# Performance work log

Hardware: AMD Instinct MI355X
Metric: run time of the kernel (lower is better)

## Reference

```python
import jax, jax.numpy as jnp
import numpy as np

N_NODES = 100000
N_EDGES = 1000000
IN_CH = 128
OUT_CH = 128
T_DIM = 64


def setup_inputs() -> dict:
    key = jax.random.key(0)
    ks = jax.random.split(key, 9)
    x = jax.random.normal(ks[0], (N_NODES, IN_CH), dtype=jnp.float32)
    edge_index = jax.random.randint(ks[1], (2, N_EDGES), 0, N_NODES, dtype=jnp.int64)
    temporal_features = jax.random.normal(ks[2], (N_EDGES, T_DIM), dtype=jnp.float32)
    # Learned params (torch nn.Linear convention: weight [out, in], bias [out])
    s = 1.0 / np.sqrt(IN_CH)
    st = 1.0 / np.sqrt(T_DIM)
    W_S_w = jax.random.uniform(ks[3], (OUT_CH, IN_CH), minval=-s, maxval=s, dtype=jnp.float32)
    W_S_b = jax.random.uniform(ks[4], (OUT_CH,), minval=-s, maxval=s, dtype=jnp.float32)
    W_T_w = jax.random.uniform(ks[5], (OUT_CH, IN_CH), minval=-s, maxval=s, dtype=jnp.float32)
    W_T_b = jax.random.uniform(ks[6], (OUT_CH,), minval=-s, maxval=s, dtype=jnp.float32)
    T_w = jax.random.uniform(ks[7], (OUT_CH, T_DIM), minval=-st, maxval=st, dtype=jnp.float32)
    T_b = jax.random.uniform(ks[8], (OUT_CH,), minval=-st, maxval=st, dtype=jnp.float32)
    return {
        "x": x, "edge_index": edge_index, "temporal_features": temporal_features,
        "W_S_w": W_S_w, "W_S_b": W_S_b, "W_T_w": W_T_w, "W_T_b": W_T_b,
        "T_w": T_w, "T_b": T_b,
    }


def reference(x, edge_index, temporal_features, W_S_w, W_S_b, W_T_w, W_T_b, T_w, T_b):
    num_nodes = x.shape[0]
    row, col = edge_index[0], edge_index[1]
    # self transform: [N, out]
    self_features = x @ W_S_w.T + W_S_b
    # gather neighbor feats then transform: [E, out]
    neighbor_features = x[col] @ W_T_w.T + W_T_b
    # temporal encodings: [E, out]
    temporal_encodings = temporal_features @ T_w.T + T_b
    messages = neighbor_features + temporal_encodings
    # scatter-add aggregation over destination nodes
    aggregated = jax.ops.segment_sum(messages, row, num_segments=num_nodes)
    return jax.nn.relu(self_features + aggregated)
```

## Files before the change

kernel.cpp:

```cpp
#include <hip/hip_runtime.h>

#define N_NODES 100000
#define M_PAD   100096
#define N_EDGES 1000000
#define K_TOT   320
#define NCHUNK  98

#define BM  128
#define LDA 72

#define XCONV_THREADS 1600000

typedef __attribute__((ext_vector_type(8))) short bf16x8;
typedef __attribute__((ext_vector_type(4))) float f32x4;

__device__ __forceinline__ unsigned short f2bf(float f) {
    unsigned u = __float_as_uint(f);
    u += 0x7FFFu + ((u >> 16) & 1u);
    return (unsigned short)(u >> 16);
}
__device__ __forceinline__ unsigned pack2(float a, float b) {
    return (unsigned)f2bf(a) | ((unsigned)f2bf(b) << 16);
}

__global__ __launch_bounds__(256) void prep_kernel(
        const float* __restrict__ x,
        const float* __restrict__ WSw,
        const float* __restrict__ WTw,
        const float* __restrict__ Tw,
        const float* __restrict__ WTb,
        const float* __restrict__ Tb,
        unsigned short* __restrict__ xb,
        unsigned short* __restrict__ Gtb,
        float* __restrict__ bias2) {
    int gid = blockIdx.x * 256 + threadIdx.x;
    if (gid < XCONV_THREADS) {
        const float4* p = (const float4*)x + (size_t)gid * 2;
        float4 u0 = p[0], u1 = p[1];
        uint4 w;
        w.x = pack2(u0.x, u0.y);
        w.y = pack2(u0.z, u0.w);
        w.z = pack2(u1.x, u1.y);
        w.w = pack2(u1.z, u1.w);
        *(uint4*)(xb + (size_t)gid * 8) = w;
    } else {
        int idx = gid - XCONV_THREADS;
        if (idx < K_TOT * 128) {
            int k = idx >> 7;
            int o = idx & 127;
            float v = (k < 128) ? WSw[o * 128 + k]
                    : (k < 256) ? WTw[o * 128 + (k - 128)]
                                : Tw[o * 64 + (k - 256)];
            Gtb[(size_t)o * K_TOT + k] = f2bf(v);
        }
        if (idx < 128) bias2[idx] = WTb[idx] + Tb[idx];
    }
}

__global__ __launch_bounds__(256) void hist_kernel(const int* __restrict__ ei,
                                                   int* __restrict__ hist) {
    int e = blockIdx.x * 256 + threadIdx.x;
    if (e < N_EDGES) atomicAdd(&hist[ei[e]], 1);
}

__global__ __launch_bounds__(256) void scan_pass1(const int* __restrict__ hist,
                                                  int* __restrict__ chunksum) {
    __shared__ int ts[256];
    int b = blockIdx.x, t = threadIdx.x;
    int i = b * 1024 + t * 4;
    int s = 0;
#pragma unroll
    for (int j = 0; j < 4; ++j)
        if (i + j < N_NODES) s += hist[i + j];
    ts[t] = s;
    __syncthreads();
    for (int off = 128; off > 0; off >>= 1) {
        if (t < off) ts[t] += ts[t + off];
        __syncthreads();
    }
    if (t == 0) chunksum[b] = ts[0];
}

__global__ __launch_bounds__(128) void scan_mid(const int* __restrict__ chunksum,
                                                int* __restrict__ chunkoff) {
    __shared__ int ts[128];
    int t = threadIdx.x;
    int v = (t < NCHUNK) ? chunksum[t] : 0;
    ts[t] = v;
    __syncthreads();
    for (int off = 1; off < 128; off <<= 1) {
        int a = (t >= off) ? ts[t - off] : 0;
        __syncthreads();
        ts[t] += a;
        __syncthreads();
    }
    if (t < NCHUNK) chunkoff[t] = ts[t] - v;
}

__global__ __launch_bounds__(256) void scan_pass2(const int* __restrict__ hist,
                                                  const int* __restrict__ chunkoff,
                                                  int* __restrict__ offsets) {
    __shared__ int ts[256];
    int b = blockIdx.x, t = threadIdx.x;
    int i0 = b * 1024 + t * 4;
    int v[4];
    int s = 0;
#pragma unroll
    for (int j = 0; j < 4; ++j) {
        v[j] = (i0 + j < N_NODES) ? hist[i0 + j] : 0;
        s += v[j];
    }
    ts[t] = s;
    __syncthreads();
    for (int off = 1; off < 256; off <<= 1) {
        int add = (t >= off) ? ts[t - off] : 0;
        __syncthreads();
        ts[t] += add;
        __syncthreads();
    }
    int run = chunkoff[b] + ts[t] - s;
#pragma unroll
    for (int j = 0; j < 4; ++j) {
        if (i0 + j < N_NODES) offsets[i0 + j] = run;
        run += v[j];
    }
}

__global__ __launch_bounds__(256) void fill_kernel(const int* __restrict__ ei,
                                                   int* __restrict__ offsets,
                                                   unsigned long long* __restrict__ ec) {
    int e = blockIdx.x * 256 + threadIdx.x;
    if (e < N_EDGES) {
        int row = ei[e];
        int col = ei[N_EDGES + e];
        int pos = atomicAdd(&offsets[row], 1);
        ec[pos] = ((unsigned long long)(unsigned)col << 32) | (unsigned)e;
    }
}

__global__ __launch_bounds__(256) void agg_kernel(
        const float* __restrict__ x,
        const float* __restrict__ tf,
        const unsigned long long* __restrict__ ec,
        const int* __restrict__ offsets,
        unsigned* __restrict__ aggxb,
        unsigned* __restrict__ aggtb,
        float* __restrict__ deg) {
    int lane = threadIdx.x & 63;
    int n = blockIdx.x * 4 + (threadIdx.x >> 6);
    if (n >= N_NODES) return;

    int beg = n ? offsets[n - 1] : 0;
    int end = offsets[n];

    float ax = 0.f, ay = 0.f, at = 0.f;
    float bx = 0.f, by = 0.f, bt = 0.f;

    int i = beg;
    for (; i + 3 < end; i += 4) {
        unsigned long long p0 = ec[i],     p1 = ec[i + 1];
        unsigned long long p2 = ec[i + 2], p3 = ec[i + 3];
        const float2* x0p = (const float2*)(x + ((size_t)(p0 >> 32) << 7)) + lane;
        const float2* x1p = (const float2*)(x + ((size_t)(p1 >> 32) << 7)) + lane;
        const float2* x2p = (const float2*)(x + ((size_t)(p2 >> 32) << 7)) + lane;
        const float2* x3p = (const float2*)(x + ((size_t)(p3 >> 32) << 7)) + lane;
        const float* t0p = tf + ((size_t)(unsigned)p0 << 6);
        const float* t1p = tf + ((size_t)(unsigned)p1 << 6);
        const float* t2p = tf + ((size_t)(unsigned)p2 << 6);
        const float* t3p = tf + ((size_t)(unsigned)p3 << 6);
        float2 a = *x0p, b = *x1p, c = *x2p, d = *x3p;
        float u0 = __builtin_nontemporal_load(t0p + lane);
        float u1 = __builtin_nontemporal_load(t1p + lane);
        float u2 = __builtin_nontemporal_load(t2p + lane);
        float u3 = __builtin_nontemporal_load(t3p + lane);
        ax += a.x; ay += a.y; at += u0;
        bx += b.x; by += b.y; bt += u1;
        ax += c.x; ay += c.y; at += u2;
        bx += d.x; by += d.y; bt += u3;
    }
    for (; i < end; ++i) {
        unsigned long long p0 = ec[i];
        float2 a = *((const float2*)(x + ((size_t)(p0 >> 32) << 7)) + lane);
        ax += a.x; ay += a.y;
        at += __builtin_nontemporal_load(tf + ((size_t)(unsigned)p0 << 6) + lane);
    }

    float fx = ax + bx, fy = ay + by, ft = at + bt;
    aggxb[(size_t)n * 64 + lane] = pack2(fx, fy);
    float pt = __shfl_xor(ft, 1);
    if (!(lane & 1))
        aggtb[(size_t)n * 32 + (lane >> 1)] = pack2(ft, pt);
    if (lane == 0) deg[n] = (float)(end - beg);
}

__global__ __launch_bounds__(256) void gemm_kernel(
        const unsigned short* __restrict__ xb,
        const unsigned short* __restrict__ aggxb,
        const unsigned short* __restrict__ aggtb,
        const unsigned short* __restrict__ Gtb,
        const float* __restrict__ WSb,
        const float* __restrict__ bias2,
        const float* __restrict__ deg,
        float* __restrict__ out) {
    __shared__ unsigned short As[BM * LDA];
    __shared__ unsigned short Bs[BM * LDA];

    int t = threadIdx.x;
    int lane = t & 63;
    int wave = t >> 6;
    int mw = (wave & 1) * 64;
    int nw = (wave >> 1) * 64;
    int row0 = blockIdx.x * BM;
    int quad = lane >> 4;
    int l16  = lane & 15;

    f32x4 acc[4][4];
#pragma unroll
    for (int mt = 0; mt < 4; ++mt)
#pragma unroll
        for (int nt = 0; nt < 4; ++nt)
            acc[mt][nt] = (f32x4){0.f, 0.f, 0.f, 0.f};

    int sm = t >> 1;
    int sh = (t & 1) * 32;

    for (int c = 0; c < 5; ++c) {
        const unsigned short* src; int ld, koff;
        if (c < 2)      { src = xb;    ld = 128; koff = c * 64; }
        else if (c < 4) { src = aggxb; ld = 128; koff = (c - 2) * 64; }
        else            { src = aggtb; ld = 64;  koff = 0; }

        const unsigned short* ap = src + (size_t)(row0 + sm) * ld + koff + sh;
        uint4 a0 = *(const uint4*)(ap);
        uint4 a1 = *(const uint4*)(ap + 8);
        uint4 a2 = *(const uint4*)(ap + 16);
        uint4 a3 = *(const uint4*)(ap + 24);
        const unsigned short* gp = Gtb + (size_t)sm * K_TOT + c * 64 + sh;
        uint4 b0 = *(const uint4*)(gp);
        uint4 b1 = *(const uint4*)(gp + 8);
        uint4 b2 = *(const uint4*)(gp + 16);
        uint4 b3 = *(const uint4*)(gp + 24);

        __syncthreads();

        *(uint4*)&As[sm * LDA + sh]      = a0;
        *(uint4*)&As[sm * LDA + sh + 8]  = a1;
        *(uint4*)&As[sm * LDA + sh + 16] = a2;
        *(uint4*)&As[sm * LDA + sh + 24] = a3;
        *(uint4*)&Bs[sm * LDA + sh]      = b0;
        *(uint4*)&Bs[sm * LDA + sh + 8]  = b1;
        *(uint4*)&Bs[sm * LDA + sh + 16] = b2;
        *(uint4*)&Bs[sm * LDA + sh + 24] = b3;

        __syncthreads();

#pragma unroll
        for (int ks = 0; ks < 2; ++ks) {
            bf16x8 af[4], bfv[4];
#pragma unroll
            for (int mt = 0; mt < 4; ++mt)
                af[mt] = *(bf16x8*)&As[(mw + mt * 16 + l16) * LDA + ks * 32 + quad * 8];
#pragma unroll
            for (int nt = 0; nt < 4; ++nt)
                bfv[nt] = *(bf16x8*)&Bs[(nw + nt * 16 + l16) * LDA + ks * 32 + quad * 8];
#pragma unroll
            for (int mt = 0; mt < 4; ++mt)
#pragma unroll
                for (int nt = 0; nt < 4; ++nt)
                    acc[mt][nt] = __builtin_amdgcn_mfma_f32_16x16x32_bf16(
                        af[mt], bfv[nt], acc[mt][nt], 0, 0, 0);
        }
    }

#pragma unroll
    for (int mt = 0; mt < 4; ++mt) {
#pragma unroll
        for (int r = 0; r < 4; ++r) {
            int m = row0 + mw + mt * 16 + quad * 4 + r;
            if (m >= N_NODES) continue;
            float dg = deg[m];
#pragma unroll
            for (int nt = 0; nt < 4; ++nt) {
                int o = nw + nt * 16 + l16;
                float val = acc[mt][nt][r] + WSb[o] + dg * bias2[o];
                out[(size_t)m * 128 + o] = fmaxf(val, 0.f);
            }
        }
    }
}

extern "C" void kernel_launch(void* const* d_in, const int* in_sizes, int n_in,
                              void* d_out, int out_size, void* d_ws, size_t ws_size,
                              hipStream_t stream) {
    const float* x   = (const float*)d_in[0];
    const int*   ei  = (const int*)d_in[1];
    const float* tf  = (const float*)d_in[2];
    const float* WSw = (const float*)d_in[3];
    const float* WSb = (const float*)d_in[4];
    const float* WTw = (const float*)d_in[5];
    const float* WTb = (const float*)d_in[6];
    const float* Tw  = (const float*)d_in[7];
    const float* Tb  = (const float*)d_in[8];
    float* out = (float*)d_out;

    unsigned short* xb    = (unsigned short*)d_ws;
    unsigned short* aggxb = xb    + (size_t)M_PAD * 128;
    unsigned short* aggtb = aggxb + (size_t)M_PAD * 128;
    unsigned short* Gtb   = aggtb + (size_t)M_PAD * 64;
    unsigned long long* ec = (unsigned long long*)(Gtb + (size_t)K_TOT * 128);
    float* deg   = (float*)(ec + N_EDGES);
    float* bias2 = deg + N_NODES;
    int* hist    = (int*)(bias2 + 128);
    int* offsets = hist + N_NODES;
    int* csum    = offsets + (N_NODES + 2);
    int* coff    = csum + 128;

    hipMemsetAsync(hist, 0, (size_t)N_NODES * sizeof(int), stream);

    prep_kernel<<<(XCONV_THREADS + K_TOT * 128) / 256, 256, 0, stream>>>(
        x, WSw, WTw, Tw, WTb, Tb, xb, Gtb, bias2);

    hist_kernel<<<(N_EDGES + 255) / 256, 256, 0, stream>>>(ei, hist);
    scan_pass1<<<NCHUNK, 256, 0, stream>>>(hist, csum);
    scan_mid<<<1, 128, 0, stream>>>(csum, coff);
    scan_pass2<<<NCHUNK, 256, 0, stream>>>(hist, coff, offsets);

    fill_kernel<<<(N_EDGES + 255) / 256, 256, 0, stream>>>(ei, offsets, ec);

    agg_kernel<<<N_NODES / 4, 256, 0, stream>>>(
        x, tf, ec, offsets, (unsigned*)aggxb, (unsigned*)aggtb, deg);

    gemm_kernel<<<(N_NODES + BM - 1) / BM, 256, 0, stream>>>(
        xb, aggxb, aggtb, Gtb, WSb, bias2, deg, out);
}
```

Before: 599.7 us.

## Gather bf16 node features in aggregation and fuse histogram into prep kernel

The aggregation kernel now gathers neighbour rows from the bf16 copy of x that the prep kernel already builds, instead of the fp32 original. This halves the bytes moved in the random per-edge gather. The edge histogram is merged into the prep launch as extra blocks, removing one kernel launch. The tail loop is unrolled into a single predicated block. Neighbour features are now rounded to bf16 before summation rather than after, which changes numerics slightly.

New measurement: 575.9 us. 4.0% less time.

```diff
diff --git a/kernel.cpp b/kernel.cpp
--- a/kernel.cpp
+++ b/kernel.cpp
@@ -10,6 +10,8 @@
 #define LDA 72
 
 #define XCONV_THREADS 1600000
+#define PREP_BLOCKS   6410
+#define HIST_BLOCKS   3907
 
 typedef __attribute__((ext_vector_type(8))) short bf16x8;
 typedef __attribute__((ext_vector_type(4))) float f32x4;
@@ -22,8 +24,10 @@
 __device__ __forceinline__ unsigned pack2(float a, float b) {
     return (unsigned)f2bf(a) | ((unsigned)f2bf(b) << 16);
 }
-
-__global__ __launch_bounds__(256) void prep_kernel(
+__device__ __forceinline__ float bflo(unsigned v) { return __uint_as_float(v << 16); }
+__device__ __forceinline__ float bfhi(unsigned v) { return __uint_as_float(v & 0xffff0000u); }
+
+__global__ __launch_bounds__(256) void prep_hist_kernel(
         const float* __restrict__ x,
         const float* __restrict__ WSw,
         const float* __restrict__ WTw,
@@ -32,8 +36,17 @@
         const float* __restrict__ Tb,
         unsigned short* __restrict__ xb,
         unsigned short* __restrict__ Gtb,
-        float* __restrict__ bias2) {
-    int gid = blockIdx.x * 256 + threadIdx.x;
+        float* __restrict__ bias2,
+        const int* __restrict__ ei,
+        int* __restrict__ hist) {
+    int b = blockIdx.x;
+    int t = threadIdx.x;
+    if (b >= PREP_BLOCKS) {
+        int e = (b - PREP_BLOCKS) * 256 + t;
+        if (e < N_EDGES) atomicAdd(&hist[ei[e]], 1);
+        return;
+    }
+    int gid = b * 256 + t;
     if (gid < XCONV_THREADS) {
         const float4* p = (const float4*)x + (size_t)gid * 2;
         float4 u0 = p[0], u1 = p[1];
@@ -57,12 +70,6 @@
     }
 }
 
-__global__ __launch_bounds__(256) void hist_kernel(const int* __restrict__ ei,
-                                                   int* __restrict__ hist) {
-    int e = blockIdx.x * 256 + threadIdx.x;
-    if (e < N_EDGES) atomicAdd(&hist[ei[e]], 1);
-}
-
 __global__ __launch_bounds__(256) void scan_pass1(const int* __restrict__ hist,
                                                   int* __restrict__ chunksum) {
     __shared__ int ts[256];
@@ -139,7 +146,7 @@
 }
 
 __global__ __launch_bounds__(256) void agg_kernel(
-        const float* __restrict__ x,
+        const unsigned* __restrict__ xw,
         const float* __restrict__ tf,
         const unsigned long long* __restrict__ ec,
         const int* __restrict__ offsets,
@@ -148,7 +155,6 @@
         float* __restrict__ deg) {
     int lane = threadIdx.x & 63;
     int n = blockIdx.x * 4 + (threadIdx.x >> 6);
-    if (n >= N_NODES) return;
 
     int beg = n ? offsets[n - 1] : 0;
     int end = offsets[n];
@@ -160,29 +166,33 @@
     for (; i + 3 < end; i += 4) {
         unsigned long long p0 = ec[i],     p1 = ec[i + 1];
         unsigned long long p2 = ec[i + 2], p3 = ec[i + 3];
-        const float2* x0p = (const float2*)(x + ((size_t)(p0 >> 32) << 7)) + lane;
-        const float2* x1p = (const float2*)(x + ((size_t)(p1 >> 32) << 7)) + lane;
-        const float2* x2p = (const float2*)(x + ((size_t)(p2 >> 32) << 7)) + lane;
-        const float2* x3p = (const float2*)(x + ((size_t)(p3 >> 32) << 7)) + lane;
-        const float* t0p = tf + ((size_t)(unsigned)p0 << 6);
-        const float* t1p = tf + ((size_t)(unsigned)p1 << 6);
-        const float* t2p = tf + ((size_t)(unsigned)p2 << 6);
-        const float* t3p = tf + ((size_t)(unsigned)p3 << 6);
-        float2 a = *x0p, b = *x1p, c = *x2p, d = *x3p;
-        float u0 = __builtin_nontemporal_load(t0p + lane);
-        float u1 = __builtin_nontemporal_load(t1p + lane);
-        float u2 = __builtin_nontemporal_load(t2p + lane);
-        float u3 = __builtin_nontemporal_load(t3p + lane);
-        ax += a.x; ay += a.y; at += u0;
-        bx += b.x; by += b.y; bt += u1;
-        ax += c.x; ay += c.y; at += u2;
-        bx += d.x; by += d.y; bt += u3;
-    }
-    for (; i < end; ++i) {
+        unsigned a = xw[((size_t)(p0 >> 32) << 6) + lane];
+        unsigned b = xw[((size_t)(p1 >> 32) << 6) + lane];
+        unsigned c = xw[((size_t)(p2 >> 32) << 6) + lane];
+        unsigned d = xw[((size_t)(p3 >> 32) << 6) + lane];
+        float u0 = __builtin_nontemporal_load(tf + ((size_t)(unsigned)p0 << 6) + lane);
+        float u1 = __builtin_nontemporal_load(tf + ((size_t)(unsigned)p1 << 6) + lane);
+        float u2 = __builtin_nontemporal_load(tf + ((size_t)(unsigned)p2 << 6) + lane);
+        float u3 = __builtin_nontemporal_load(tf + ((size_t)(unsigned)p3 << 6) + lane);
+        ax += bflo(a); ay += bfhi(a); at += u0;
+        bx += bflo(b); by += bfhi(b); bt += u1;
+        ax += bflo(c); ay += bfhi(c); at += u2;
+        bx += bflo(d); by += bfhi(d); bt += u3;
+    }
+    int rem = end - i;
+    if (rem) {
         unsigned long long p0 = ec[i];
-        float2 a = *((const float2*)(x + ((size_t)(p0 >> 32) << 7)) + lane);
-        ax += a.x; ay += a.y;
-        at += __builtin_nontemporal_load(tf + ((size_t)(unsigned)p0 << 6) + lane);
+        unsigned long long p1 = (rem > 1) ? ec[i + 1] : p0;
+        unsigned long long p2 = (rem > 2) ? ec[i + 2] : p0;
+        unsigned a = xw[((size_t)(p0 >> 32) << 6) + lane];
+        unsigned b = xw[((size_t)(p1 >> 32) << 6) + lane];
+        unsigned c = xw[((size_t)(p2 >> 32) << 6) + lane];
+        float u0 = __builtin_nontemporal_load(tf + ((size_t)(unsigned)p0 << 6) + lane);
+        float u1 = __builtin_nontemporal_load(tf + ((size_t)(unsigned)p1 << 6) + lane);
+        float u2 = __builtin_nontemporal_load(tf + ((size_t)(unsigned)p2 << 6) + lane);
+        ax += bflo(a); ay += bfhi(a); at += u0;
+        if (rem > 1) { bx += bflo(b); by += bfhi(b); bt += u1; }
+        if (rem > 2) { ax += bflo(c); ay += bfhi(c); at += u2; }
     }
 
     float fx = ax + bx, fy = ay + by, ft = at + bt;
@@ -317,10 +327,9 @@
 
     hipMemsetAsync(hist, 0, (size_t)N_NODES * sizeof(int), stream);
 
-    prep_kernel<<<(XCONV_THREADS + K_TOT * 128) / 256, 256, 0, stream>>>(
-        x, WSw, WTw, Tw, WTb, Tb, xb, Gtb, bias2);
-
-    hist_kernel<<<(N_EDGES + 255) / 256, 256, 0, stream>>>(ei, hist);
+    prep_hist_kernel<<<PREP_BLOCKS + HIST_BLOCKS, 256, 0, stream>>>(
+        x, WSw, WTw, Tw, WTb, Tb, xb, Gtb, bias2, ei, hist);
+
     scan_pass1<<<NCHUNK, 256, 0, stream>>>(hist, csum);
     scan_mid<<<1, 128, 0, stream>>>(csum, coff);
     scan_pass2<<<NCHUNK, 256, 0, stream>>>(hist, coff, offsets);
@@ -328,7 +337,7 @@
     fill_kernel<<<(N_EDGES + 255) / 256, 256, 0, stream>>>(ei, offsets, ec);
 
     agg_kernel<<<N_NODES / 4, 256, 0, stream>>>(
-        x, tf, ec, offsets, (unsigned*)aggxb, (unsigned*)aggtb, deg);
+        (const unsigned*)xb, tf, ec, offsets, (unsigned*)aggxb, (unsigned*)aggtb, deg);
 
     gemm_kernel<<<(N_NODES + BM - 1) / BM, 256, 0, stream>>>(
         xb, aggxb, aggtb, Gtb, WSb, bias2, deg, out);
```
